# Optimization experiments

Hardware: AMD Instinct MI355X
Metric: run time of the kernel (lower is better)

## Reference

```python
import jax, jax.numpy as jnp
import numpy as np

CONV_NUM = 8
CONV_SIZE = 96
HIDDEN = 768  # = CONV_NUM * CONV_SIZE
MAX_LEN = 128


def get_entity(x, s, e):
    # x: [B, L, H]; mean of x[i, s[i]:max(e[i], s[i]+1)] per sample (ragged gather+mean)
    e = jnp.maximum(e, s + 1)
    pos = jnp.arange(x.shape[1])  # [L]
    mask = (pos[None, :] >= s[:, None]) & (pos[None, :] < e[:, None])  # [B, L]
    m = mask.astype(x.dtype)
    return jnp.einsum('blh,bl->bh', x, m) / jnp.sum(m, axis=1, keepdims=True)


def feature_abstract(head_ent, tail_ent, x, fc_W, fc_b):
    # head_ent/tail_ent: [B, HIDDEN] -> per-sample conv filters; x: [B, HIDDEN]
    B = x.shape[0]
    wh = head_ent.reshape(B * CONV_NUM, 1, 1, CONV_SIZE)
    wt = tail_ent.reshape(B * CONV_NUM, 1, 1, CONV_SIZE)
    lhs = x.reshape(1, B, 1, HIDDEN)  # NCHW, groups=B -> per-sample correlation
    h = jax.nn.relu(jax.lax.conv_general_dilated(lhs, wh, (1, 1), 'VALID', feature_group_count=B))
    t = jax.nn.relu(jax.lax.conv_general_dilated(lhs, wt, (1, 1), 'VALID', feature_group_count=B))
    # h,t: [1, B*CONV_NUM, 1, T] with T = HIDDEN - CONV_SIZE + 1
    ht = jnp.concatenate([h, t], axis=3).reshape(B * CONV_NUM, -1)  # [B*cn, 2T]
    ht = ht.reshape(B * CONV_NUM, -1, 2).mean(axis=-1)  # AvgPool1d(k=2, s=2) -> [B*cn, T]
    flat = ht.reshape(B, -1)  # [B, cn*T] (dropout is identity in eval)
    return flat @ fc_W.T + fc_b  # [B, HIDDEN]


def setup_inputs() -> dict:
    key = jax.random.key(0)
    ks = jax.random.split(key, 16)
    Bs, Bq, L, H = 400, 1200, MAX_LEN, HIDDEN

    def spans(k1, k2, B):
        s = jax.random.randint(k1, (B,), 0, 100)
        e = jnp.minimum(s + jax.random.randint(k2, (B,), 1, 20), L)
        return s.astype(jnp.int64), e.astype(jnp.int64)

    s_eh, s_eh_end = spans(ks[0], ks[1], Bs)
    s_et, s_et_end = spans(ks[2], ks[3], Bs)
    q_eh, q_eh_end = spans(ks[4], ks[5], Bq)
    q_et, q_et_end = spans(ks[6], ks[7], Bq)
    fc_in = (H - CONV_SIZE + 1) * CONV_NUM  # 5384
    return {
        'all_support': jax.random.normal(ks[8], (Bs, L, H), jnp.float32),
        'support_emb': jax.random.normal(ks[9], (Bs, H), jnp.float32),
        'all_query': jax.random.normal(ks[10], (Bq, L, H), jnp.float32),
        'query_emb': jax.random.normal(ks[11], (Bq, H), jnp.float32),
        'fc_W': jax.random.normal(ks[12], (H, fc_in), jnp.float32) / np.sqrt(fc_in),
        'fc_b': jnp.zeros((H,), jnp.float32),
        's_eh': s_eh, 's_eh_end': s_eh_end, 's_et': s_et, 's_et_end': s_et_end,
        'q_eh': q_eh, 'q_eh_end': q_eh_end, 'q_et': q_et, 'q_et_end': q_et_end,
        'N': 10, 'K': 5, 'total_Q': 150,
    }


def reference(all_support, support_emb, all_query, query_emb, fc_W, fc_b,
              s_eh, s_eh_end, s_et, s_et_end, q_eh, q_eh_end, q_et, q_et_end,
              N, K, total_Q):
    sh = get_entity(all_support, s_eh, s_eh_end)
    st = get_entity(all_support, s_et, s_et_end)
    qh = get_entity(all_query, q_eh, q_eh_end)
    qt = get_entity(all_query, q_et, q_et_end)

    sup = feature_abstract(sh, st, support_emb, fc_W, fc_b).reshape(-1, N, K, HIDDEN)
    qry = feature_abstract(qh, qt, query_emb, fc_W, fc_b).reshape(-1, total_Q, HIDDEN)

    proto = sup.mean(axis=2)  # [Be, N, H]
    # -||proto - query||^2 over feature dim -> [Be, total_Q, N]
    diff = proto[:, None, :, :] - qry[:, :, None, :]
    logits = -jnp.sum(diff * diff, axis=-1)
    minn = logits.min(axis=-1)
    logits = jnp.concatenate([logits, minn[..., None] - 1.0], axis=2)  # [Be, total_Q, N+1]
    pred = jnp.argmax(logits.reshape(-1, N + 1), axis=1)
    return logits, pred
```

## Files before the change

### kernel.cpp

```cpp
#include <hip/hip_runtime.h>

#define H        768
#define LMAX     128
#define CONV_NUM 8
#define CONV_SIZE 96
#define T_CONV   673
#define FC_IN    5384
#define KP       5408
#define KSTEPS   (KP / 32)
#define N_WAY    10
#define K_SHOT   5
#define TOTAL_Q  150
#define SPLITK   8
#define BS       400
#define BQ       1200
#define MTOT     1600
#define NPROTO   80
#define MA       1280

using s16x8 = __attribute__((ext_vector_type(8))) short;
using f32x4 = __attribute__((ext_vector_type(4))) float;
typedef unsigned short u16;

__device__ __forceinline__ u16 f2bf(float x) {
    unsigned u = __float_as_uint(x);
    u += 0x7FFFu + ((u >> 16) & 1u);
    return (u16)(u >> 16);
}
__device__ __forceinline__ float bf2f(u16 b) { return __uint_as_float(((unsigned)b) << 16); }

__device__ __forceinline__ void gl16(const u16* g, u16* l) {
    __builtin_amdgcn_global_load_lds(
        (const __attribute__((address_space(1))) unsigned int*)g,
        (__attribute__((address_space(3))) unsigned int*)l, 16, 0, 0);
}

#define HTS 678
#define XCS 784
__global__ __launch_bounds__(256, 4) void pre_kernel(
    const float* __restrict__ all_support, const float* __restrict__ all_query,
    const float* __restrict__ support_emb, const float* __restrict__ query_emb,
    const float* __restrict__ fc_W,
    const int* __restrict__ s_eh, const int* __restrict__ s_eh_end,
    const int* __restrict__ s_et, const int* __restrict__ s_et_end,
    const int* __restrict__ q_eh, const int* __restrict__ q_eh_end,
    const int* __restrict__ q_et, const int* __restrict__ q_et_end,
    u16* __restrict__ flatS, u16* __restrict__ A_bf,
    u16* __restrict__ Wh)
{
    int bid = blockIdx.x;
    int tid = threadIdx.x;

    if (bid >= MTOT) {
        int r = bid - MTOT;
        const float* wr = fc_W + (size_t)r * FC_IN;
        u16* whr = Wh + (size_t)r * KP;
        for (int j4 = tid; j4 < KP / 4; j4 += 256) {
            int j = j4 * 4;
            ushort4 o;
            if (j4 < FC_IN / 4) {
                float4 v = *(const float4*)(wr + j);
                o.x = f2bf(v.x); o.y = f2bf(v.y); o.z = f2bf(v.z); o.w = f2bf(v.w);
            } else {
                o.x = 0; o.y = 0; o.z = 0; o.w = 0;
            }
            *(ushort4*)(whr + j) = o;
        }
        return;
    }

    __shared__ u16 htb[16 * HTS];
    __shared__ u16 filt_h[16 * 96];
    __shared__ u16 filt_l[16 * 96];
    __shared__ u16 xcs[8][XCS];

    int b = bid;
    const float* src;
    int sh, eh, st, et;
    if (b < BS) {
        src = all_support + (size_t)b * LMAX * H;
        sh = s_eh[b]; eh = s_eh_end[b]; st = s_et[b]; et = s_et_end[b];
    } else {
        int m = b - BS;
        src = all_query + (size_t)m * LMAX * H;
        sh = q_eh[m]; eh = q_eh_end[m]; st = q_et[m]; et = q_et_end[m];
    }
    if (eh < sh + 1) eh = sh + 1;
    if (et < st + 1) et = st + 1;

    {
        float a0 = 0.f, a1 = 0.f, a2 = 0.f, b0 = 0.f, b1 = 0.f, b2 = 0.f;
        float c0 = 0.f, c1 = 0.f, c2 = 0.f, d0 = 0.f, d1 = 0.f, d2 = 0.f;
        int r = sh;
        for (; r + 4 <= eh; r += 4) {
            const float* p0 = src + (size_t)r * H;
            const float* p1 = p0 + H;
            const float* p2 = p0 + 2 * H;
            const float* p3 = p0 + 3 * H;
            a0 += p0[tid]; a1 += p0[tid + 256]; a2 += p0[tid + 512];
            b0 += p1[tid]; b1 += p1[tid + 256]; b2 += p1[tid + 512];
            c0 += p2[tid]; c1 += p2[tid + 256]; c2 += p2[tid + 512];
            d0 += p3[tid]; d1 += p3[tid + 256]; d2 += p3[tid + 512];
        }
        for (; r < eh; ++r) {
            const float* p0 = src + (size_t)r * H;
            a0 += p0[tid]; a1 += p0[tid + 256]; a2 += p0[tid + 512];
        }
        float rc = 1.0f / (float)(eh - sh);
        float m0 = ((a0 + b0) + (c0 + d0)) * rc;
        float m1 = ((a1 + b1) + (c1 + d1)) * rc;
        float m2 = ((a2 + b2) + (c2 + d2)) * rc;
        u16 h0 = f2bf(m0), h1 = f2bf(m1), h2 = f2bf(m2);
        filt_h[tid] = h0;       filt_l[tid] = f2bf(m0 - bf2f(h0));
        filt_h[tid + 256] = h1; filt_l[tid + 256] = f2bf(m1 - bf2f(h1));
        filt_h[tid + 512] = h2; filt_l[tid + 512] = f2bf(m2 - bf2f(h2));
        a0 = a1 = a2 = b0 = b1 = b2 = c0 = c1 = c2 = d0 = d1 = d2 = 0.f;
        r = st;
        for (; r + 4 <= et; r += 4) {
            const float* p0 = src + (size_t)r * H;
            const float* p1 = p0 + H;
            const float* p2 = p0 + 2 * H;
            const float* p3 = p0 + 3 * H;
            a0 += p0[tid]; a1 += p0[tid + 256]; a2 += p0[tid + 512];
            b0 += p1[tid]; b1 += p1[tid + 256]; b2 += p1[tid + 512];
            c0 += p2[tid]; c1 += p2[tid + 256]; c2 += p2[tid + 512];
            d0 += p3[tid]; d1 += p3[tid + 256]; d2 += p3[tid + 512];
        }
        for (; r < et; ++r) {
            const float* p0 = src + (size_t)r * H;
            a0 += p0[tid]; a1 += p0[tid + 256]; a2 += p0[tid + 512];
        }
        rc = 1.0f / (float)(et - st);
        m0 = ((a0 + b0) + (c0 + d0)) * rc;
        m1 = ((a1 + b1) + (c1 + d1)) * rc;
        m2 = ((a2 + b2) + (c2 + d2)) * rc;
        h0 = f2bf(m0); h1 = f2bf(m1); h2 = f2bf(m2);
        filt_h[tid + 768] = h0;  filt_l[tid + 768] = f2bf(m0 - bf2f(h0));
        filt_h[tid + 1024] = h1; filt_l[tid + 1024] = f2bf(m1 - bf2f(h1));
        filt_h[tid + 1280] = h2; filt_l[tid + 1280] = f2bf(m2 - bf2f(h2));
    }

    {
        if (tid < 192) {
            int row = tid / 24, idx = tid % 24;
            int j = 768 - row + idx;
            if (j < XCS) xcs[row][j] = 0;
        }
        if (tid >= 192 && tid < 192 + 80) {
            int t = tid - 192;
            htb[(t / 5) * HTS + 673 + (t % 5)] = 0;
        }
        const float* xsrc = (b < BS) ? (support_emb + (size_t)b * H)
                                     : (query_emb + (size_t)(b - BS) * H);
        if (tid < 192) {
            float4 v = *(const float4*)(xsrc + tid * 4);
            u16 h[4] = {f2bf(v.x), f2bf(v.y), f2bf(v.z), f2bf(v.w)};
            #pragma unroll
            for (int u = 0; u < 4; ++u) {
                int i = tid * 4 + u;
                #pragma unroll
                for (int c = 0; c < 8; ++c)
                    if (i >= c) xcs[c][i - c] = h[u];
            }
        }
    }
    __syncthreads();

    {
        int lane = tid & 63, wv = tid >> 6;
        int n = lane & 15, g = lane >> 4;
        int afo = n * 96 + g * 8;
        s16x8 fh0 = *(const s16x8*)&filt_h[afo];
        s16x8 fh1 = *(const s16x8*)&filt_h[afo + 32];
        s16x8 fh2 = *(const s16x8*)&filt_h[afo + 64];
        s16x8 fl0 = *(const s16x8*)&filt_l[afo];
        s16x8 fl1 = *(const s16x8*)&filt_l[afo + 32];
        s16x8 fl2 = *(const s16x8*)&filt_l[afo + 64];
        const u16* xrow = &xcs[n & 7][g * 8 + (n & 8)];
        #pragma unroll 1
        for (int nt = wv; nt < 43; nt += 4) {
            const u16* xp = xrow + nt * 16;
            s16x8 x0 = *(const s16x8*)(xp);
            s16x8 x1 = *(const s16x8*)(xp + 32);
            s16x8 x2 = *(const s16x8*)(xp + 64);
            f32x4 a = (f32x4){0.f, 0.f, 0.f, 0.f};
            a = __builtin_amdgcn_mfma_f32_16x16x32_bf16(fh0, x0, a, 0, 0, 0);
            a = __builtin_amdgcn_mfma_f32_16x16x32_bf16(fl0, x0, a, 0, 0, 0);
            a = __builtin_amdgcn_mfma_f32_16x16x32_bf16(fh1, x1, a, 0, 0, 0);
            a = __builtin_amdgcn_mfma_f32_16x16x32_bf16(fl1, x1, a, 0, 0, 0);
            a = __builtin_amdgcn_mfma_f32_16x16x32_bf16(fh2, x2, a, 0, 0, 0);
            a = __builtin_amdgcn_mfma_f32_16x16x32_bf16(fl2, x2, a, 0, 0, 0);
            int pcol = nt * 16 + n;
            if (pcol < T_CONV) {
                #pragma unroll
                for (int r = 0; r < 4; ++r)
                    htb[(g * 4 + r) * HTS + pcol] = f2bf(fmaxf(a[r], 0.f));
            }
        }
    }
    __syncthreads();

    u16* oh = (b < BS) ? (flatS + (size_t)b * KP)
                       : (A_bf + (size_t)(NPROTO + b - BS) * KP);
    for (int t = tid; t < KP / 8; t += 256) {
        int i0 = t * 8;
        s16x8 o;
        if (i0 < FC_IN) {
            #pragma unroll
            for (int u = 0; u < 8; ++u) {
                int i = i0 + u;
                int f = (int)(((unsigned)i * 24929u) >> 24);
                int j = i - f * 673;
                int e0 = 2 * j, e1 = 2 * j + 1;
                float v0 = bf2f((e0 < T_CONV) ? htb[f * HTS + e0]
                                              : htb[(8 + f) * HTS + (e0 - T_CONV)]);
                float v1 = bf2f((e1 < T_CONV) ? htb[f * HTS + e1]
                                              : htb[(8 + f) * HTS + (e1 - T_CONV)]);
                o[u] = (short)f2bf(0.5f * (v0 + v1));
            }
        } else {
            #pragma unroll
            for (int u = 0; u < 8; ++u) o[u] = 0;
        }
        *(s16x8*)(oh + i0) = o;
    }
}

__global__ __launch_bounds__(256) void avg_kernel(
    const u16* __restrict__ flatS, u16* __restrict__ A_bf)
{
    int i = blockIdx.x;
    int q = blockIdx.y;
    size_t base = (size_t)i * K_SHOT * KP;
    int t = threadIdx.x;
    if (t >= 169) return;
    int j = (q * 169 + t) * 8;
    float s[8] = {0.f, 0.f, 0.f, 0.f, 0.f, 0.f, 0.f, 0.f};
    #pragma unroll
    for (int k = 0; k < K_SHOT; ++k) {
        s16x8 vh = *(const s16x8*)(flatS + base + (size_t)k * KP + j);
        #pragma unroll
        for (int u = 0; u < 8; ++u)
            s[u] += bf2f((u16)vh[u]);
    }
    s16x8 oh;
    #pragma unroll
    for (int u = 0; u < 8; ++u)
        oh[u] = (short)f2bf(s[u] * (1.0f / K_SHOT));
    *(s16x8*)(A_bf + (size_t)i * KP + j) = oh;
}

#define ASEG 8192
#define BSEG 4096
#define BUFU (ASEG + BSEG)

#define STAGE(ks, buf) do {                                     \
    int kb_ = (ks) * 32;                                        \
    u16* L_ = &lds[buf][0];                                     \
    gl16(Ah_g + aoff0 + kb_, L_ + cA0 * 8);                     \
    gl16(Ah_g + aoff1 + kb_, L_ + cA1 * 8);                     \
    gl16(Ah_g + aoff2 + kb_, L_ + cA2 * 8);                     \
    gl16(Ah_g + aoff3 + kb_, L_ + cA3 * 8);                     \
    gl16(Bh_g + boff0 + kb_, L_ + ASEG + cB0 * 8);              \
    gl16(Bh_g + boff1 + kb_, L_ + ASEG + cB1 * 8);              \
} while (0)

__global__ __launch_bounds__(256, 2) void gemm_mfma(
    const u16* __restrict__ Ah_g, const u16* __restrict__ Bh_g,
    u16* __restrict__ partsB)
{
    __shared__ u16 lds[2][BUFU];

    int tid = threadIdx.x;
    int wg = (blockIdx.x & 7) * 30 + (blockIdx.x >> 3);
    int sk = wg / 30;
    int rem = wg % 30;
    int n0 = (rem / 5) * 128;
    int m0 = (rem % 5) * 256;

    int ks0 = (KSTEPS * sk) / SPLITK;
    int nk = (KSTEPS * (sk + 1)) / SPLITK - ks0;

    int cA0 = tid, cA1 = tid + 256, cA2 = tid + 512, cA3 = tid + 768;
    int cB0 = tid, cB1 = tid + 256;
    size_t aoff0 = (size_t)(m0 + (cA0 >> 6) * 16 + (cA0 & 15)) * KP + ((cA0 >> 4) & 3) * 8;
    size_t aoff1 = (size_t)(m0 + (cA1 >> 6) * 16 + (cA1 & 15)) * KP + ((cA1 >> 4) & 3) * 8;
    size_t aoff2 = (size_t)(m0 + (cA2 >> 6) * 16 + (cA2 & 15)) * KP + ((cA2 >> 4) & 3) * 8;
    size_t aoff3 = (size_t)(m0 + (cA3 >> 6) * 16 + (cA3 & 15)) * KP + ((cA3 >> 4) & 3) * 8;
    size_t boff0 = (size_t)(n0 + (cB0 >> 6) * 16 + (cB0 & 15)) * KP + ((cB0 >> 4) & 3) * 8;
    size_t boff1 = (size_t)(n0 + (cB1 >> 6) * 16 + (cB1 & 15)) * KP + ((cB1 >> 4) & 3) * 8;

    int w = tid >> 6, lane = tid & 63;
    int lfr = ((lane >> 4) * 16 + (lane & 15)) * 8;

    f32x4 acc[4][8];
    #pragma unroll
    for (int i = 0; i < 4; ++i)
        #pragma unroll
        for (int j = 0; j < 8; ++j) acc[i][j] = (f32x4){0.f, 0.f, 0.f, 0.f};

    STAGE(ks0, 0);
    STAGE(ks0 + 1, 1);

    int cur = 0;
    for (int k = 0; k < nk; ++k) {
        if (k + 1 < nk) asm volatile("s_waitcnt vmcnt(6)" ::: "memory");
        else            asm volatile("s_waitcnt vmcnt(0)" ::: "memory");
        __builtin_amdgcn_s_barrier();

        const u16* L = &lds[cur][0];
        s16x8 ah[4], bh[8];
        #pragma unroll
        for (int f = 0; f < 4; ++f)
            ah[f] = *(const s16x8*)(L + (w * 4 + f) * 512 + lfr);
        #pragma unroll
        for (int j = 0; j < 8; ++j)
            bh[j] = *(const s16x8*)(L + ASEG + j * 512 + lfr);
        asm volatile("s_waitcnt lgkmcnt(0)" ::: "memory");
        __builtin_amdgcn_s_barrier();

        if (k + 2 < nk) STAGE(ks0 + k + 2, cur);

        #pragma unroll
        for (int i = 0; i < 4; ++i)
            #pragma unroll
            for (int j = 0; j < 8; ++j)
                acc[i][j] = __builtin_amdgcn_mfma_f32_16x16x32_bf16(ah[i], bh[j], acc[i][j], 0, 0, 0);
        cur ^= 1;
    }

    int rbase = m0 + w * 64 + (lane >> 4) * 4;
    int cbase = n0 + (lane & 15);
    #pragma unroll
    for (int i = 0; i < 4; ++i) {
        int row0 = rbase + i * 16;
        #pragma unroll
        for (int j = 0; j < 8; ++j) {
            int col = cbase + j * 16;
            u16* dst = partsB + ((size_t)sk * MA + row0) * H + col;
            #pragma unroll
            for (int r = 0; r < 4; ++r)
                dst[(size_t)r * H] = f2bf(acc[i][j][r]);
        }
    }
}

__global__ __launch_bounds__(256) void protofin_kernel(
    const u16* __restrict__ partsB, float* __restrict__ proto)
{
    int i = blockIdx.x;
    int tid = threadIdx.x;
    if (tid >= 192) return;
    int d0 = tid * 4;
    float s0 = 0.f, s1 = 0.f, s2 = 0.f, s3 = 0.f;
    #pragma unroll
    for (int sp = 0; sp < SPLITK; ++sp) {
        ushort4 v = *(const ushort4*)(partsB + ((size_t)sp * MA + i) * H + d0);
        s0 += bf2f(v.x); s1 += bf2f(v.y); s2 += bf2f(v.z); s3 += bf2f(v.w);
    }
    *(float4*)(proto + (size_t)i * H + d0) = make_float4(s0, s1, s2, s3);
}

__global__ __launch_bounds__(256) void dist_kernel(
    const u16* __restrict__ partsB, const float* __restrict__ proto,
    float* __restrict__ outp)
{
    int bid = blockIdx.x;
    int e = bid / TOTAL_Q;
    int tid = threadIdx.x;
    int m = NPROTO + bid;
    int d0 = tid * 4;

    float qv0 = 0.f, qv1 = 0.f, qv2 = 0.f, qv3 = 0.f;
    if (tid < 192) {
        #pragma unroll
        for (int sp = 0; sp < SPLITK; ++sp) {
            ushort4 v = *(const ushort4*)(partsB + ((size_t)sp * MA + m) * H + d0);
            qv0 += bf2f(v.x); qv1 += bf2f(v.y); qv2 += bf2f(v.z); qv3 += bf2f(v.w);
        }
    }

    __shared__ float red[N_WAY][4];
    __shared__ float lvals[N_WAY];
    int wave = tid >> 6, lane = tid & 63;
    for (int n = 0; n < N_WAY; ++n) {
        float p = 0.f;
        if (tid < 192) {
            const float* pr = proto + (size_t)(e * N_WAY + n) * H + d0;
            float4 pv = *(const float4*)pr;
            float df0 = pv.x - qv0, df1 = pv.y - qv1, df2 = pv.z - qv2, df3 = pv.w - qv3;
            p = df0 * df0;
            p = fmaf(df1, df1, p);
            p = fmaf(df2, df2, p);
            p = fmaf(df3, df3, p);
        }
        #pragma unroll
        for (int off = 32; off > 0; off >>= 1)
            p += __shfl_down(p, off);
        if (lane == 0) red[n][wave] = p;
    }
    __syncthreads();
    if (tid < N_WAY) {
        float v = red[tid][0] + red[tid][1] + red[tid][2] + red[tid][3];
        lvals[tid] = -v;
        outp[(size_t)bid * (N_WAY + 1) + tid] = -v;
    }
    __syncthreads();
    if (tid == 0) {
        float mn = lvals[0];
        #pragma unroll
        for (int n = 1; n < N_WAY; ++n) mn = fminf(mn, lvals[n]);
        float last = mn - 1.0f;
        outp[(size_t)bid * (N_WAY + 1) + N_WAY] = last;
        float best = lvals[0];
        int bi = 0;
        for (int n = 1; n < N_WAY; ++n)
            if (lvals[n] > best) { best = lvals[n]; bi = n; }
        if (last > best) bi = N_WAY;
        outp[(size_t)BQ * (N_WAY + 1) + bid] = (float)bi;
    }
}

extern "C" void kernel_launch(void* const* d_in, const int* in_sizes, int n_in,
                              void* d_out, int out_size, void* d_ws, size_t ws_size,
                              hipStream_t stream)
{
    const float* all_support = (const float*)d_in[0];
    const float* support_emb = (const float*)d_in[1];
    const float* all_query   = (const float*)d_in[2];
    const float* query_emb   = (const float*)d_in[3];
    const float* fc_W        = (const float*)d_in[4];
    const int* s_eh     = (const int*)d_in[6];
    const int* s_eh_end = (const int*)d_in[7];
    const int* s_et     = (const int*)d_in[8];
    const int* s_et_end = (const int*)d_in[9];
    const int* q_eh     = (const int*)d_in[10];
    const int* q_eh_end = (const int*)d_in[11];
    const int* q_et     = (const int*)d_in[12];
    const int* q_et_end = (const int*)d_in[13];

    u16* partsB  = (u16*)d_ws;
    float* proto = (float*)(partsB + (size_t)SPLITK * MA * H);
    u16* Wh      = (u16*)(proto + (size_t)NPROTO * H);
    u16* A_bf    = Wh + (size_t)H * KP;
    u16* flatS   = A_bf + (size_t)MA * KP;

    pre_kernel<<<MTOT + H, 256, 0, stream>>>(
        all_support, all_query, support_emb, query_emb, fc_W,
        s_eh, s_eh_end, s_et, s_et_end, q_eh, q_eh_end, q_et, q_et_end,
        flatS, A_bf, Wh);

    avg_kernel<<<dim3(NPROTO, 4), 256, 0, stream>>>(flatS, A_bf);

    gemm_mfma<<<240, 256, 0, stream>>>(A_bf, Wh, partsB);

    protofin_kernel<<<NPROTO, 256, 0, stream>>>(partsB, proto);

    dist_kernel<<<BQ, 256, 0, stream>>>(partsB, proto, (float*)d_out);
}
```

Measured before the change: 69.57 us.

## Shrink GEMM tile to 128x128 with 2x2 waves and double the grid

The split-K MFMA GEMM tile drops from 256x128 to 128x128, with the four waves now arranged 2x2 so each computes 64x64. The grid grows from 240 to 480 workgroups and the launch bound rises to 3 workgroups per CU, which halves LDS per block and the accumulator registers per thread. The aim is to fill the 256 CUs better and raise occupancy, at the cost of less operand reuse per tile and more global/LDS traffic per FLOP. The avg, protofin and dist kernels also switch to launch sizes that match their active thread counts, so idle threads are no longer launched.

```diff
diff --git a/kernel.cpp b/kernel.cpp
--- a/kernel.cpp
+++ b/kernel.cpp
@@ -230,11 +230,10 @@
     const u16* __restrict__ flatS, u16* __restrict__ A_bf)
 {
     int i = blockIdx.x;
-    int q = blockIdx.y;
+    int t = blockIdx.y * 256 + threadIdx.x;
+    if (t >= KP / 8) return;
     size_t base = (size_t)i * K_SHOT * KP;
-    int t = threadIdx.x;
-    if (t >= 169) return;
-    int j = (q * 169 + t) * 8;
+    int j = t * 8;
     float s[8] = {0.f, 0.f, 0.f, 0.f, 0.f, 0.f, 0.f, 0.f};
     #pragma unroll
     for (int k = 0; k < K_SHOT; ++k) {
@@ -250,7 +249,7 @@
     *(s16x8*)(A_bf + (size_t)i * KP + j) = oh;
 }
 
-#define ASEG 8192
+#define ASEG 4096
 #define BSEG 4096
 #define BUFU (ASEG + BSEG)
 
@@ -259,63 +258,58 @@
     u16* L_ = &lds[buf][0];                                     \
     gl16(Ah_g + aoff0 + kb_, L_ + cA0 * 8);                     \
     gl16(Ah_g + aoff1 + kb_, L_ + cA1 * 8);                     \
-    gl16(Ah_g + aoff2 + kb_, L_ + cA2 * 8);                     \
-    gl16(Ah_g + aoff3 + kb_, L_ + cA3 * 8);                     \
-    gl16(Bh_g + boff0 + kb_, L_ + ASEG + cB0 * 8);              \
-    gl16(Bh_g + boff1 + kb_, L_ + ASEG + cB1 * 8);              \
+    gl16(Bh_g + boff0 + kb_, L_ + ASEG + cA0 * 8);              \
+    gl16(Bh_g + boff1 + kb_, L_ + ASEG + cA1 * 8);              \
 } while (0)
 
-__global__ __launch_bounds__(256, 2) void gemm_mfma(
+__global__ __launch_bounds__(256, 3) void gemm_mfma(
     const u16* __restrict__ Ah_g, const u16* __restrict__ Bh_g,
     u16* __restrict__ partsB)
 {
     __shared__ u16 lds[2][BUFU];
 
     int tid = threadIdx.x;
-    int wg = (blockIdx.x & 7) * 30 + (blockIdx.x >> 3);
-    int sk = wg / 30;
-    int rem = wg % 30;
-    int n0 = (rem / 5) * 128;
-    int m0 = (rem % 5) * 256;
+    int wg = (blockIdx.x & 7) * 60 + (blockIdx.x >> 3);
+    int sk = wg / 60;
+    int rem = wg % 60;
+    int n0 = (rem / 10) * 128;
+    int m0 = (rem % 10) * 128;
 
     int ks0 = (KSTEPS * sk) / SPLITK;
     int nk = (KSTEPS * (sk + 1)) / SPLITK - ks0;
 
-    int cA0 = tid, cA1 = tid + 256, cA2 = tid + 512, cA3 = tid + 768;
-    int cB0 = tid, cB1 = tid + 256;
+    int cA0 = tid, cA1 = tid + 256;
     size_t aoff0 = (size_t)(m0 + (cA0 >> 6) * 16 + (cA0 & 15)) * KP + ((cA0 >> 4) & 3) * 8;
     size_t aoff1 = (size_t)(m0 + (cA1 >> 6) * 16 + (cA1 & 15)) * KP + ((cA1 >> 4) & 3) * 8;
-    size_t aoff2 = (size_t)(m0 + (cA2 >> 6) * 16 + (cA2 & 15)) * KP + ((cA2 >> 4) & 3) * 8;
-    size_t aoff3 = (size_t)(m0 + (cA3 >> 6) * 16 + (cA3 & 15)) * KP + ((cA3 >> 4) & 3) * 8;
-    size_t boff0 = (size_t)(n0 + (cB0 >> 6) * 16 + (cB0 & 15)) * KP + ((cB0 >> 4) & 3) * 8;
-    size_t boff1 = (size_t)(n0 + (cB1 >> 6) * 16 + (cB1 & 15)) * KP + ((cB1 >> 4) & 3) * 8;
+    size_t boff0 = (size_t)(n0 + (cA0 >> 6) * 16 + (cA0 & 15)) * KP + ((cA0 >> 4) & 3) * 8;
+    size_t boff1 = (size_t)(n0 + (cA1 >> 6) * 16 + (cA1 & 15)) * KP + ((cA1 >> 4) & 3) * 8;
 
     int w = tid >> 6, lane = tid & 63;
+    int wm = w >> 1, wn = w & 1;
     int lfr = ((lane >> 4) * 16 + (lane & 15)) * 8;
 
-    f32x4 acc[4][8];
+    f32x4 acc[4][4];
     #pragma unroll
     for (int i = 0; i < 4; ++i)
         #pragma unroll
-        for (int j = 0; j < 8; ++j) acc[i][j] = (f32x4){0.f, 0.f, 0.f, 0.f};
+        for (int j = 0; j < 4; ++j) acc[i][j] = (f32x4){0.f, 0.f, 0.f, 0.f};
 
     STAGE(ks0, 0);
     STAGE(ks0 + 1, 1);
 
     int cur = 0;
     for (int k = 0; k < nk; ++k) {
-        if (k + 1 < nk) asm volatile("s_waitcnt vmcnt(6)" ::: "memory");
+        if (k + 1 < nk) asm volatile("s_waitcnt vmcnt(4)" ::: "memory");
         else            asm volatile("s_waitcnt vmcnt(0)" ::: "memory");
         __builtin_amdgcn_s_barrier();
 
         const u16* L = &lds[cur][0];
-        s16x8 ah[4], bh[8];
-        #pragma unroll
-        for (int f = 0; f < 4; ++f)
-            ah[f] = *(const s16x8*)(L + (w * 4 + f) * 512 + lfr);
-        #pragma unroll
-        for (int j = 0; j < 8; ++j)
-            bh[j] = *(const s16x8*)(L + ASEG + j * 512 + lfr);
+        s16x8 ah[4], bh[4];
+        #pragma unroll
+        for (int f = 0; f < 4; ++f) {
+            ah[f] = *(const s16x8*)(L + (wm * 4 + f) * 512 + lfr);
+            bh[f] = *(const s16x8*)(L + ASEG + (wn * 4 + f) * 512 + lfr);
+        }
         asm volatile("s_waitcnt lgkmcnt(0)" ::: "memory");
         __builtin_amdgcn_s_barrier();
 
@@ -324,18 +318,18 @@
         #pragma unroll
         for (int i = 0; i < 4; ++i)
             #pragma unroll
-            for (int j = 0; j < 8; ++j)
+            for (int j = 0; j < 4; ++j)
                 acc[i][j] = __builtin_amdgcn_mfma_f32_16x16x32_bf16(ah[i], bh[j], acc[i][j], 0, 0, 0);
         cur ^= 1;
     }
 
-    int rbase = m0 + w * 64 + (lane >> 4) * 4;
-    int cbase = n0 + (lane & 15);
+    int rbase = m0 + wm * 64 + (lane >> 4) * 4;
+    int cbase = n0 + wn * 64 + (lane & 15);
     #pragma unroll
     for (int i = 0; i < 4; ++i) {
         int row0 = rbase + i * 16;
         #pragma unroll
-        for (int j = 0; j < 8; ++j) {
+        for (int j = 0; j < 4; ++j) {
             int col = cbase + j * 16;
             u16* dst = partsB + ((size_t)sk * MA + row0) * H + col;
             #pragma unroll
@@ -345,13 +339,11 @@
     }
 }
 
-__global__ __launch_bounds__(256) void protofin_kernel(
+__global__ __launch_bounds__(192) void protofin_kernel(
     const u16* __restrict__ partsB, float* __restrict__ proto)
 {
     int i = blockIdx.x;
-    int tid = threadIdx.x;
-    if (tid >= 192) return;
-    int d0 = tid * 4;
+    int d0 = threadIdx.x * 4;
     float s0 = 0.f, s1 = 0.f, s2 = 0.f, s3 = 0.f;
     #pragma unroll
     for (int sp = 0; sp < SPLITK; ++sp) {
@@ -361,7 +353,7 @@
     *(float4*)(proto + (size_t)i * H + d0) = make_float4(s0, s1, s2, s3);
 }
 
-__global__ __launch_bounds__(256) void dist_kernel(
+__global__ __launch_bounds__(192) void dist_kernel(
     const u16* __restrict__ partsB, const float* __restrict__ proto,
     float* __restrict__ outp)
 {
@@ -372,28 +364,23 @@
     int d0 = tid * 4;
 
     float qv0 = 0.f, qv1 = 0.f, qv2 = 0.f, qv3 = 0.f;
-    if (tid < 192) {
-        #pragma unroll
-        for (int sp = 0; sp < SPLITK; ++sp) {
-            ushort4 v = *(const ushort4*)(partsB + ((size_t)sp * MA + m) * H + d0);
-            qv0 += bf2f(v.x); qv1 += bf2f(v.y); qv2 += bf2f(v.z); qv3 += bf2f(v.w);
-        }
-    }
-
-    __shared__ float red[N_WAY][4];
+    #pragma unroll
+    for (int sp = 0; sp < SPLITK; ++sp) {
+        ushort4 v = *(const ushort4*)(partsB + ((size_t)sp * MA + m) * H + d0);
+        qv0 += bf2f(v.x); qv1 += bf2f(v.y); qv2 += bf2f(v.z); qv3 += bf2f(v.w);
+    }
+
+    __shared__ float red[N_WAY][3];
     __shared__ float lvals[N_WAY];
     int wave = tid >> 6, lane = tid & 63;
     for (int n = 0; n < N_WAY; ++n) {
-        float p = 0.f;
-        if (tid < 192) {
-            const float* pr = proto + (size_t)(e * N_WAY + n) * H + d0;
-            float4 pv = *(const float4*)pr;
-            float df0 = pv.x - qv0, df1 = pv.y - qv1, df2 = pv.z - qv2, df3 = pv.w - qv3;
-            p = df0 * df0;
-            p = fmaf(df1, df1, p);
-            p = fmaf(df2, df2, p);
-            p = fmaf(df3, df3, p);
-        }
+        const float* pr = proto + (size_t)(e * N_WAY + n) * H + d0;
+        float4 pv = *(const float4*)pr;
+        float df0 = pv.x - qv0, df1 = pv.y - qv1, df2 = pv.z - qv2, df3 = pv.w - qv3;
+        float p = df0 * df0;
+        p = fmaf(df1, df1, p);
+        p = fmaf(df2, df2, p);
+        p = fmaf(df3, df3, p);
         #pragma unroll
         for (int off = 32; off > 0; off >>= 1)
             p += __shfl_down(p, off);
@@ -401,7 +388,7 @@
     }
     __syncthreads();
     if (tid < N_WAY) {
-        float v = red[tid][0] + red[tid][1] + red[tid][2] + red[tid][3];
+        float v = red[tid][0] + red[tid][1] + red[tid][2];
         lvals[tid] = -v;
         outp[(size_t)bid * (N_WAY + 1) + tid] = -v;
     }
@@ -450,11 +437,11 @@
         s_eh, s_eh_end, s_et, s_et_end, q_eh, q_eh_end, q_et, q_et_end,
         flatS, A_bf, Wh);
 
-    avg_kernel<<<dim3(NPROTO, 4), 256, 0, stream>>>(flatS, A_bf);
-
-    gemm_mfma<<<240, 256, 0, stream>>>(A_bf, Wh, partsB);
-
-    protofin_kernel<<<NPROTO, 256, 0, stream>>>(partsB, proto);
-
-    dist_kernel<<<BQ, 256, 0, stream>>>(partsB, proto, (float*)d_out);
-}
+    avg_kernel<<<dim3(NPROTO, 3), 256, 0, stream>>>(flatS, A_bf);
+
+    gemm_mfma<<<480, 256, 0, stream>>>(A_bf, Wh, partsB);
+
+    protofin_kernel<<<NPROTO, 192, 0, stream>>>(partsB, proto);
+
+    dist_kernel<<<BQ, 192, 0, stream>>>(partsB, proto, (float*)d_out);
+}
```

Measured after the change: 68.74 us. Within noise of the previous version (-1.2%).
